# Performance work log

Measured on AMD Instinct MI355X. Metric: run time of the kernel, lower is better.

Reference implementation:

```python
import jax, jax.numpy as jnp
import numpy as np

NUM_NODES = 100000
NUM_EDGES = 1600000
NUM_GRAPHS = 512
HIDDEN = 128
LAYERS = 3
NUM_CLASSES = 10
BN_EPS = 1e-5


def setup_inputs() -> dict:
    key = jax.random.key(0)
    ks = jax.random.split(key, 12)
    x = jax.random.normal(ks[0], (NUM_NODES, HIDDEN), dtype=jnp.float32)
    edge_index = jax.random.randint(ks[1], (2, NUM_EDGES), 0, NUM_NODES, dtype=jnp.int32)
    batch = jnp.sort(jax.random.randint(ks[2], (NUM_NODES,), 0, NUM_GRAPHS, dtype=jnp.int32))
    s = 1.0 / np.sqrt(HIDDEN)
    W1 = jax.random.normal(ks[3], (LAYERS, HIDDEN, HIDDEN), dtype=jnp.float32) * s
    b1 = jnp.zeros((LAYERS, HIDDEN), dtype=jnp.float32)
    W2 = jax.random.normal(ks[4], (LAYERS, HIDDEN, HIDDEN), dtype=jnp.float32) * s
    b2 = jnp.zeros((LAYERS, HIDDEN), dtype=jnp.float32)
    gamma = jnp.ones((LAYERS, HIDDEN), dtype=jnp.float32)
    beta = jnp.zeros((LAYERS, HIDDEN), dtype=jnp.float32)
    eps_gin = jnp.zeros((LAYERS,), dtype=jnp.float32)  # train_eps init 0
    lin1_w = jax.random.normal(ks[5], (LAYERS * HIDDEN, HIDDEN), dtype=jnp.float32) * (1.0 / np.sqrt(LAYERS * HIDDEN))
    lin1_b = jnp.zeros((HIDDEN,), dtype=jnp.float32)
    lin2_w = jax.random.normal(ks[6], (HIDDEN, NUM_CLASSES), dtype=jnp.float32) * s
    lin2_b = jnp.zeros((NUM_CLASSES,), dtype=jnp.float32)
    return {"x": x, "edge_index": edge_index, "batch": batch,
            "W1": W1, "b1": b1, "W2": W2, "b2": b2,
            "gamma": gamma, "beta": beta, "eps_gin": eps_gin,
            "lin1_w": lin1_w, "lin1_b": lin1_b, "lin2_w": lin2_w, "lin2_b": lin2_b}


def _batchnorm(h, g, b):
    mu = jnp.mean(h, axis=0, keepdims=True)
    var = jnp.var(h, axis=0, keepdims=True)
    return (h - mu) * jax.lax.rsqrt(var + BN_EPS) * g + b


def reference(x, edge_index, batch, W1, b1, W2, b2, gamma, beta, eps_gin,
              lin1_w, lin1_b, lin2_w, lin2_b):
    src, dst = edge_index[0], edge_index[1]
    n = x.shape[0]
    h = x
    layer_hs = []
    for l in range(LAYERS):
        # scatter-add neighbor aggregation: agg[i] = sum_{j->i} h[j]
        agg = jax.ops.segment_sum(h[src], dst, num_segments=n)
        z = (1.0 + eps_gin[l]) * h + agg
        z = jax.nn.relu(z @ W1[l] + b1[l])
        z = jax.nn.relu(z @ W2[l] + b2[l])
        h = _batchnorm(z, gamma[l], beta[l])
        layer_hs.append(h)
    h_cat = jnp.concatenate(layer_hs, axis=-1)  # [N, LAYERS*HIDDEN]
    # global mean pool per graph
    sums = jax.ops.segment_sum(h_cat, batch, num_segments=NUM_GRAPHS)
    counts = jax.ops.segment_sum(jnp.ones((n, 1), h_cat.dtype), batch, num_segments=NUM_GRAPHS)
    g = sums / jnp.maximum(counts, 1.0)
    g = jax.nn.relu(g @ lin1_w + lin1_b)
    # dropout is identity in inference
    return g @ lin2_w + lin2_b
```

## Files before the change

### kernel.cpp

```cpp
#include <hip/hip_runtime.h>

#define HID 128
#define NGRAPH 512
#define NLAYERS 3
#define BN_EPS 1e-5f
#define NPB 256
#define EB 4096

typedef __attribute__((ext_vector_type(8))) short bf16x8;
typedef __attribute__((ext_vector_type(4))) float f32x4;
typedef __attribute__((ext_vector_type(2))) float f32x2;

__device__ inline unsigned short f2bf(float x) {
    union { float f; unsigned u; } v; v.f = x;
    unsigned r = v.u + 0x7FFFu + ((v.u >> 16) & 1u);
    return (unsigned short)(r >> 16);
}
__device__ inline float bf2f(unsigned short b) {
    union { float f; unsigned u; } v; v.u = ((unsigned)b) << 16; return v.f;
}
__device__ inline f32x2 bfp(unsigned u) {
    union { unsigned q; float f; } lo, hi;
    lo.q = u << 16; hi.q = u & 0xFFFF0000u;
    f32x2 r; r[0] = lo.f; r[1] = hi.f; return r;
}

__global__ void k_prep(float* __restrict__ ssliced, float* __restrict__ gsum,
                       const float4* __restrict__ x4, ushort* __restrict__ xb, int total4,
                       const float* __restrict__ W1, ushort* __restrict__ w1h, ushort* __restrict__ w1l,
                       const float* __restrict__ W2, ushort* __restrict__ w2h, ushort* __restrict__ w2l,
                       int wtotal, int xblocks,
                       const int* __restrict__ dst, int E, int* __restrict__ blkcnt) {
    __shared__ int hist[512];
    int b = blockIdx.x, t = threadIdx.x;
    if (b < 768) {
        if (b < 24) ssliced[b * 256 + t] = 0.0f;
        gsum[b * 256 + t] = 0.0f;
    } else if (b < 1152) {
        int gid = (b - 768) * 256 + t;
        const float* W; ushort *Wh, *Wl; int e;
        if (gid < wtotal) { W = W1; Wh = w1h; Wl = w1l; e = gid; }
        else              { W = W2; Wh = w2h; Wl = w2l; e = gid - wtotal; }
        if (e < wtotal) {
            int l = e >> 14, rem = e & 16383, k = rem >> 7, n = rem & 127;
            float v = W[e];
            ushort hi = f2bf(v);
            ushort lo = f2bf(v - bf2f(hi));
            int o = (l << 14) + (n << 7) + k;
            Wh[o] = hi; Wl[o] = lo;
        }
    } else if (b < 1152 + xblocks) {
        int i = (b - 1152) * 256 + t;
        if (i < total4) {
            float4 v = x4[i];
            uint2 p;
            p.x = ((unsigned)f2bf(v.y) << 16) | f2bf(v.x);
            p.y = ((unsigned)f2bf(v.w) << 16) | f2bf(v.z);
            ((uint2*)xb)[i] = p;
        }
    } else {
        int b2 = b - (1152 + xblocks);
        hist[t] = 0; hist[t + 256] = 0;
        __syncthreads();
        int base = b2 * EB;
        #pragma unroll
        for (int i = 0; i < 16; ++i) {
            int e = base + i * 256 + t;
            if (e < E) atomicAdd(&hist[dst[e] >> 8], 1);
        }
        __syncthreads();
        blkcnt[b2 * 512 + t]       = hist[t];
        blkcnt[b2 * 512 + t + 256] = hist[t + 256];
    }
}

__global__ __launch_bounds__(256) void k_btot_reduce(const int* __restrict__ blkcnt,
                                                     int eblk, int* __restrict__ tot) {
    __shared__ int sh[256];
    int b = blockIdx.x;
    int t = threadIdx.x;
    int s = 0;
    for (int j = t; j < eblk; j += 256) s += blkcnt[j * 512 + b];
    sh[t] = s;
    __syncthreads();
    #pragma unroll
    for (int k = 128; k > 0; k >>= 1) {
        if (t < k) sh[t] += sh[t + k];
        __syncthreads();
    }
    if (t == 0) tot[b] = sh[0];
}

__global__ __launch_bounds__(512) void k_bscan(const int* __restrict__ tot, int nb, int E,
                                               int* __restrict__ bbase, int* __restrict__ rowptrN) {
    __shared__ int sh[512];
    int t = threadIdx.x;
    sh[t] = (t < nb) ? tot[t] : 0;
    __syncthreads();
    #pragma unroll
    for (int s = 1; s < 512; s <<= 1) {
        int v = (t >= s) ? sh[t - s] : 0;
        __syncthreads();
        sh[t] += v;
        __syncthreads();
    }
    if (t < nb) bbase[t] = (t == 0) ? 0 : sh[t - 1];
    if (t == 0) { bbase[nb] = E; *rowptrN = E; }
}

__global__ __launch_bounds__(512) void k_colscan(int* __restrict__ blkcnt, int eblk,
                                                 const int* __restrict__ bbase) {
    __shared__ int sh[512];
    int t = threadIdx.x;
    int b = blockIdx.x;
    sh[t] = (t < eblk) ? blkcnt[t * 512 + b] : 0;
    __syncthreads();
    #pragma unroll
    for (int s = 1; s < 512; s <<= 1) {
        int v = (t >= s) ? sh[t - s] : 0;
        __syncthreads();
        sh[t] += v;
        __syncthreads();
    }
    int excl = (t == 0) ? 0 : sh[t - 1];
    if (t < eblk) blkcnt[t * 512 + b] = bbase[b] + excl;
}

__global__ __launch_bounds__(256) void k_bscatter(const int* __restrict__ src,
                                                  const int* __restrict__ dst, int E,
                                                  const int* __restrict__ blkcnt,
                                                  unsigned* __restrict__ pairs) {
    __shared__ int hist[512];
    __shared__ int lbase[512];
    int t = threadIdx.x;
    hist[t] = 0; hist[t + 256] = 0;
    lbase[t]       = blkcnt[blockIdx.x * 512 + t];
    lbase[t + 256] = blkcnt[blockIdx.x * 512 + t + 256];
    __syncthreads();
    int base = blockIdx.x * EB;
    #pragma unroll
    for (int i = 0; i < 16; ++i) {
        int e = base + i * 256 + t;
        if (e < E) {
            int d = dst[e];
            int b = d >> 8;
            int pos = lbase[b] + atomicAdd(&hist[b], 1);
            pairs[pos] = ((unsigned)(d & 255) << 24) | (unsigned)src[e];
        }
    }
}

__global__ __launch_bounds__(256) void k_bbuild(const unsigned* __restrict__ pairs,
                                                const int* __restrict__ bbase, int N,
                                                int* __restrict__ rowptr, int* __restrict__ csr) {
    __shared__ int cnt[256];
    __shared__ int off[256];
    int t = threadIdx.x;
    int b = blockIdx.x;
    int base = bbase[b], bcount = bbase[b + 1] - base;
    cnt[t] = 0;
    __syncthreads();
    for (int i = t; i < bcount; i += 256) atomicAdd(&cnt[pairs[base + i] >> 24], 1);
    __syncthreads();
    off[t] = cnt[t];
    __syncthreads();
    for (int s = 1; s < 256; s <<= 1) {
        int v = (t >= s) ? off[t - s] : 0;
        __syncthreads();
        off[t] += v;
        __syncthreads();
    }
    int excl = (t == 0) ? 0 : off[t - 1];
    int node = b * NPB + t;
    if (node < N) rowptr[node] = base + excl;
    cnt[t] = excl;
    __syncthreads();
    for (int i = t; i < bcount; i += 256) {
        unsigned p = pairs[base + i];
        int dl = p >> 24;
        int pos = base + atomicAdd(&cnt[dl], 1);
        csr[pos] = (int)(p & 0xFFFFFFu);
    }
}

__global__ __launch_bounds__(256, 8) void k_agg(
        const int* __restrict__ rowptr, const int* __restrict__ csr_src,
        const uint2* __restrict__ hinb,
        const float* __restrict__ prev_stats,
        const float* __restrict__ g_row, const float* __restrict__ be_row,
        const float* __restrict__ eps_gin, int layer,
        ushort* __restrict__ z0out, int N) {
    const int t = threadIdx.x;
    const int lane = t & 63;
    const int wv = t >> 6;
    const int q = lane >> 4;
    const int f = lane & 15;

    f32x2 scv2[4], shv2[4];
    if (prev_stats) {
        float invn = 1.0f / (float)N;
        #pragma unroll
        for (int d = 0; d < 4; ++d) {
            #pragma unroll
            for (int h = 0; h < 2; ++h) {
                int fi = f * 8 + d * 2 + h;
                float mu = prev_stats[fi] * invn;
                float var = prev_stats[128 + fi] * invn - mu * mu;
                float inv = rsqrtf(var + BN_EPS);
                float scj = g_row[fi] * inv;
                scv2[d][h] = scj; shv2[d][h] = be_row[fi] - mu * scj;
            }
        }
    } else {
        #pragma unroll
        for (int d = 0; d < 4; ++d) { scv2[d] = (f32x2){1.f, 1.f}; shv2[d] = (f32x2){0.f, 0.f}; }
    }
    float e1 = 1.0f + eps_gin[layer];
    const uint4* hin4 = (const uint4*)hinb;

    int r = blockIdx.x * 16 + wv * 4 + q;
    f32x2 a2[4];
    #pragma unroll
    for (int d = 0; d < 4; ++d) a2[d] = (f32x2){0.f, 0.f};
    float cdeg = 0.f;
    if (r < N) {
        int beg = rowptr[r], end = rowptr[r + 1];
        uint4 hv = hin4[(size_t)r * 16 + f];
        a2[0] = e1 * bfp(hv.x); a2[1] = e1 * bfp(hv.y);
        a2[2] = e1 * bfp(hv.z); a2[3] = e1 * bfp(hv.w);
        int p = beg;
        for (; p + 8 <= end; p += 8) {
            int s0 = csr_src[p],     s1 = csr_src[p + 1], s2 = csr_src[p + 2], s3 = csr_src[p + 3];
            int s4 = csr_src[p + 4], s5 = csr_src[p + 5], s6 = csr_src[p + 6], s7 = csr_src[p + 7];
            uint4 v0 = hin4[(size_t)s0 * 16 + f];
            uint4 v1 = hin4[(size_t)s1 * 16 + f];
            uint4 v2 = hin4[(size_t)s2 * 16 + f];
            uint4 v3 = hin4[(size_t)s3 * 16 + f];
            uint4 v4 = hin4[(size_t)s4 * 16 + f];
            uint4 v5 = hin4[(size_t)s5 * 16 + f];
            uint4 v6 = hin4[(size_t)s6 * 16 + f];
            uint4 v7 = hin4[(size_t)s7 * 16 + f];
            a2[0] += ((bfp(v0.x) + bfp(v1.x)) + (bfp(v2.x) + bfp(v3.x)))
                   + ((bfp(v4.x) + bfp(v5.x)) + (bfp(v6.x) + bfp(v7.x)));
            a2[1] += ((bfp(v0.y) + bfp(v1.y)) + (bfp(v2.y) + bfp(v3.y)))
                   + ((bfp(v4.y) + bfp(v5.y)) + (bfp(v6.y) + bfp(v7.y)));
            a2[2] += ((bfp(v0.z) + bfp(v1.z)) + (bfp(v2.z) + bfp(v3.z)))
                   + ((bfp(v4.z) + bfp(v5.z)) + (bfp(v6.z) + bfp(v7.z)));
            a2[3] += ((bfp(v0.w) + bfp(v1.w)) + (bfp(v2.w) + bfp(v3.w)))
                   + ((bfp(v4.w) + bfp(v5.w)) + (bfp(v6.w) + bfp(v7.w)));
        }
        if (p < end) {
            int last = end - 1;
            int c1 = min(p + 1, last), c2 = min(p + 2, last), c3 = min(p + 3, last);
            int c4 = min(p + 4, last), c5 = min(p + 5, last), c6 = min(p + 6, last);
            int s0 = csr_src[p],  s1 = csr_src[c1], s2 = csr_src[c2], s3 = csr_src[c3];
            int s4 = csr_src[c4], s5 = csr_src[c5], s6 = csr_src[c6];
            uint4 v0 = hin4[(size_t)s0 * 16 + f];
            uint4 v1 = hin4[(size_t)s1 * 16 + f];
            uint4 v2 = hin4[(size_t)s2 * 16 + f];
            uint4 v3 = hin4[(size_t)s3 * 16 + f];
            uint4 v4 = hin4[(size_t)s4 * 16 + f];
            uint4 v5 = hin4[(size_t)s5 * 16 + f];
            uint4 v6 = hin4[(size_t)s6 * 16 + f];
            int rem = end - p;
            unsigned m1 = (rem > 1) ? 0xFFFFFFFFu : 0u;
            unsigned m2 = (rem > 2) ? 0xFFFFFFFFu : 0u;
            unsigned m3 = (rem > 3) ? 0xFFFFFFFFu : 0u;
            unsigned m4 = (rem > 4) ? 0xFFFFFFFFu : 0u;
            unsigned m5 = (rem > 5) ? 0xFFFFFFFFu : 0u;
            unsigned m6 = (rem > 6) ? 0xFFFFFFFFu : 0u;
            a2[0] += ((bfp(v0.x) + bfp(v1.x & m1)) + (bfp(v2.x & m2) + bfp(v3.x & m3)))
                   + ((bfp(v4.x & m4) + bfp(v5.x & m5)) + bfp(v6.x & m6));
            a2[1] += ((bfp(v0.y) + bfp(v1.y & m1)) + (bfp(v2.y & m2) + bfp(v3.y & m3)))
                   + ((bfp(v4.y & m4) + bfp(v5.y & m5)) + bfp(v6.y & m6));
            a2[2] += ((bfp(v0.z) + bfp(v1.z & m1)) + (bfp(v2.z & m2) + bfp(v3.z & m3)))
                   + ((bfp(v4.z & m4) + bfp(v5.z & m5)) + bfp(v6.z & m6));
            a2[3] += ((bfp(v0.w) + bfp(v1.w & m1)) + (bfp(v2.w & m2) + bfp(v3.w & m3)))
                   + ((bfp(v4.w & m4) + bfp(v5.w & m5)) + bfp(v6.w & m6));
        }
        cdeg = e1 + (float)(end - beg);
    }
    f32x2 rr2[4];
    #pragma unroll
    for (int d = 0; d < 4; ++d) rr2[d] = scv2[d] * a2[d] + cdeg * shv2[d];
    uint4 ph;
    ph.x = ((unsigned)f2bf(rr2[0][1]) << 16) | f2bf(rr2[0][0]);
    ph.y = ((unsigned)f2bf(rr2[1][1]) << 16) | f2bf(rr2[1][0]);
    ph.z = ((unsigned)f2bf(rr2[2][1]) << 16) | f2bf(rr2[2][0]);
    ph.w = ((unsigned)f2bf(rr2[3][1]) << 16) | f2bf(rr2[3][0]);
    if (r < N) ((uint4*)z0out)[(size_t)r * 16 + f] = ph;
}

__global__ __launch_bounds__(256, 2) void k_mlp_dense(
        const uint4* __restrict__ z0, int layer, const int* __restrict__ batch,
        const ushort* __restrict__ w1h, const ushort* __restrict__ w1l,
        const float* __restrict__ b1,
        const ushort* __restrict__ w2h, const ushort* __restrict__ w2l,
        const float* __restrict__ b2,
        ushort* __restrict__ Hout, float* __restrict__ stat_sl,
        float* __restrict__ gsum, int N, int ntiles) {
    __shared__ __align__(16) ushort smem[8192];
    const int t = threadIdx.x;
    const int lane = t & 63;
    const int wv = t >> 6;
    const int li = lane & 15;
    const int kq = lane >> 4;
    const int n0 = wv * 32;
    const int swz = (li & 7) * 4;

    bf16x8 w1hr[8], w1lr[8], w2hr[8], w2lr[8];
    #pragma unroll
    for (int ch = 0; ch < 2; ++ch)
        #pragma unroll
        for (int ks = 0; ks < 2; ++ks)
            #pragma unroll
            for (int nt = 0; nt < 2; ++nt) {
                int i = ch * 4 + ks * 2 + nt;
                size_t wo = (size_t)(n0 + nt * 16 + li) * 128 + (ch * 64 + ks * 32 + kq * 8);
                w1hr[i] = *(const bf16x8*)&w1h[wo];
                w1lr[i] = *(const bf16x8*)&w1l[wo];
                w2hr[i] = *(const bf16x8*)&w2h[wo];
                w2lr[i] = *(const bf16x8*)&w2l[wo];
            }
    float bz0 = b1[n0 + li], bz1 = b1[n0 + 16 + li];
    float bb0 = b2[n0 + li], bb1 = b2[n0 + 16 + li];

    for (int tile = blockIdx.x; tile < ntiles; tile += gridDim.x) {
        const int row0 = tile * 64;

        {
            const uint4 zz = {0u, 0u, 0u, 0u};
            #pragma unroll
            for (int i = 0; i < 4; ++i) {
                int idx = i * 256 + t;
                int r = idx >> 4, f = idx & 15;
                uint4 v = (row0 + r < N) ? z0[(size_t)(row0 + r) * 16 + f] : zz;
                ((uint4*)smem)[r * 16 + (f ^ (r & 7))] = v;
            }
        }
        __syncthreads();

        f32x4 acc[4][2];
        #pragma unroll
        for (int i = 0; i < 4; ++i) {
            acc[i][0] = (f32x4){0.f, 0.f, 0.f, 0.f};
            acc[i][1] = (f32x4){0.f, 0.f, 0.f, 0.f};
        }

        #pragma unroll
        for (int ch = 0; ch < 2; ++ch) {
            #pragma unroll
            for (int ks = 0; ks < 2; ++ks) {
                int kcol = ch * 8 + ks * 4 + kq;
                #pragma unroll
                for (int mt = 0; mt < 4; ++mt) {
                    int r = mt * 16 + li;
                    int hw = (r * 16 + (kcol ^ (li & 7))) * 8;
                    bf16x8 ah = *(const bf16x8*)&smem[hw];
                    #pragma unroll
                    for (int nt = 0; nt < 2; ++nt) {
                        int i = ch * 4 + ks * 2 + nt;
                        acc[mt][nt] = __builtin_amdgcn_mfma_f32_16x16x32_bf16(ah, w1hr[i], acc[mt][nt], 0, 0, 0);
                        acc[mt][nt] = __builtin_amdgcn_mfma_f32_16x16x32_bf16(ah, w1lr[i], acc[mt][nt], 0, 0, 0);
                    }
                }
            }
        }

        __syncthreads();
        #pragma unroll
        for (int mt = 0; mt < 4; ++mt) {
            #pragma unroll
            for (int nt = 0; nt < 2; ++nt) {
                int c = n0 + nt * 16 + li;
                int dk = c >> 1;
                int halfbase = (dk >> 5) * 32;
                int dlow = dk & 31;
                int codd = c & 1;
                float bias = nt ? bz1 : bz0;
                #pragma unroll
                for (int reg = 0; reg < 4; ++reg) {
                    int r = mt * 16 + kq * 4 + reg;
                    float v = fmaxf(acc[mt][nt][reg] + bias, 0.f);
                    int us = (r * 64 + halfbase + (dlow ^ ((r & 7) * 4))) * 2 + codd;
                    smem[us] = f2bf(v);
                }
            }
        }
        #pragma unroll
        for (int i = 0; i < 4; ++i) {
            acc[i][0] = (f32x4){0.f, 0.f, 0.f, 0.f};
            acc[i][1] = (f32x4){0.f, 0.f, 0.f, 0.f};
        }
        __syncthreads();

        #pragma unroll
        for (int ch = 0; ch < 2; ++ch) {
            #pragma unroll
            for (int ks = 0; ks < 2; ++ks) {
                int aoff = (ks * 16 + kq * 4) ^ swz;
                #pragma unroll
                for (int mt = 0; mt < 4; ++mt) {
                    int idx = ((mt * 16 + li) * 64 + ch * 32 + aoff) * 2;
                    bf16x8 ah = *(const bf16x8*)&smem[idx];
                    #pragma unroll
                    for (int nt = 0; nt < 2; ++nt) {
                        int i = ch * 4 + ks * 2 + nt;
                        acc[mt][nt] = __builtin_amdgcn_mfma_f32_16x16x32_bf16(ah, w2hr[i], acc[mt][nt], 0, 0, 0);
                        acc[mt][nt] = __builtin_amdgcn_mfma_f32_16x16x32_bf16(ah, w2lr[i], acc[mt][nt], 0, 0, 0);
                    }
                }
            }
        }

        int btr[4][4];
        #pragma unroll
        for (int mt = 0; mt < 4; ++mt)
            #pragma unroll
            for (int reg = 0; reg < 4; ++reg) {
                int grow = row0 + mt * 16 + kq * 4 + reg;
                btr[mt][reg] = (grow < N) ? batch[grow] : -1;
            }
        __syncthreads();
        float s0 = 0.f, q0 = 0.f, s1 = 0.f, q1 = 0.f;
        #pragma unroll
        for (int mt = 0; mt < 4; ++mt) {
            #pragma unroll
            for (int reg = 0; reg < 4; ++reg) {
                int r = mt * 16 + kq * 4 + reg;
                float v0 = fmaxf(acc[mt][0][reg] + bb0, 0.f);
                float v1 = fmaxf(acc[mt][1][reg] + bb1, 0.f);
                smem[r * 128 + n0 + li]      = f2bf(v0);
                smem[r * 128 + n0 + 16 + li] = f2bf(v1);
                if (btr[mt][reg] >= 0) {
                    s0 += v0; q0 += v0 * v0; s1 += v1; q1 += v1 * v1;
                }
            }
        }
        __syncthreads();
        {
            int valid = N - row0; if (valid > 64) valid = 64;
            int tot = valid * 16;
            for (int i = t; i < tot; i += 256) {
                int r = i >> 4, c = i & 15;
                ((uint4*)&Hout[(size_t)(row0 + r) * HID])[c] = ((const uint4*)smem)[r * 16 + c];
            }
        }
        s0 += __shfl_xor(s0, 16); s0 += __shfl_xor(s0, 32);
        q0 += __shfl_xor(q0, 16); q0 += __shfl_xor(q0, 32);
        s1 += __shfl_xor(s1, 16); s1 += __shfl_xor(s1, 32);
        q1 += __shfl_xor(q1, 16); q1 += __shfl_xor(q1, 32);
        if (kq == 0) {
            float* ss = stat_sl + (blockIdx.x & 7) * 768;
            unsafeAtomicAdd(&ss[n0 + li], s0);
            unsafeAtomicAdd(&ss[128 + n0 + li], q0);
            unsafeAtomicAdd(&ss[n0 + 16 + li], s1);
            unsafeAtomicAdd(&ss[128 + n0 + 16 + li], q1);
        }
        int lastr = N - 1; if (lastr > row0 + 63) lastr = row0 + 63;
        int g_lo = batch[row0], g_hi = batch[lastr];
        int loff = layer * HID;
        for (int g = g_lo; g <= g_hi; ++g) {
            float p0 = 0.f, p1 = 0.f;
            #pragma unroll
            for (int mt = 0; mt < 4; ++mt)
                #pragma unroll
                for (int reg = 0; reg < 4; ++reg) {
                    if (btr[mt][reg] == g) {
                        p0 += fmaxf(acc[mt][0][reg] + bb0, 0.f);
                        p1 += fmaxf(acc[mt][1][reg] + bb1, 0.f);
                    }
                }
            p0 += __shfl_xor(p0, 16); p0 += __shfl_xor(p0, 32);
            p1 += __shfl_xor(p1, 16); p1 += __shfl_xor(p1, 32);
            if (kq == 0) {
                unsafeAtomicAdd(&gsum[(size_t)g * 384 + loff + n0 + li], p0);
                unsafeAtomicAdd(&gsum[(size_t)g * 384 + loff + n0 + 16 + li], p1);
            }
        }
        __syncthreads();
    }
}

__global__ __launch_bounds__(256) void k_sfold(const float* __restrict__ sliced,
                                               float* __restrict__ out) {
    int t = threadIdx.x;
    float s = 0.f;
    #pragma unroll
    for (int k = 0; k < 8; ++k) s += sliced[k * 768 + t];
    out[t] = s;
}

__global__ __launch_bounds__(128) void k_mlp(const int* __restrict__ batch, int N,
                     const float* __restrict__ gsum, const float* __restrict__ stats,
                     const float* __restrict__ gamma, const float* __restrict__ beta,
                     const float* __restrict__ w1, const float* __restrict__ b1,
                     const float* __restrict__ w2, const float* __restrict__ b2,
                     float* __restrict__ out) {
    __shared__ float gl[8][384];
    __shared__ float hh[8][128];
    int g0 = blockIdx.x * 8, t = threadIdx.x;
    float invn = 1.0f / (float)N;
    float sc[NLAYERS], sh[NLAYERS];
    #pragma unroll
    for (int l = 0; l < NLAYERS; ++l) {
        float mu = stats[l * 256 + t] * invn;
        float var = stats[l * 256 + 128 + t] * invn - mu * mu;
        float inv = rsqrtf(var + BN_EPS);
        sc[l] = gamma[l * HID + t] * inv;
        sh[l] = beta[l * HID + t] - mu * sc[l];
    }
    for (int j = 0; j < 8; ++j) {
        int g = g0 + j;
        int start, end;
        { int lo = 0, hi = N; while (lo < hi) { int m = (lo + hi) >> 1; if (batch[m] < g) lo = m + 1; else hi = m; } start = lo; }
        { int lo = start, hi = N; while (lo < hi) { int m = (lo + hi) >> 1; if (batch[m] < g + 1) lo = m + 1; else hi = m; } end = lo; }
        float cnt = (float)(end - start);
        float invc = 1.0f / fmaxf(cnt, 1.0f);
        #pragma unroll
        for (int l = 0; l < NLAYERS; ++l)
            gl[j][l * 128 + t] = (gsum[(size_t)g * 384 + l * 128 + t] * sc[l] + sh[l] * cnt) * invc;
    }
    __syncthreads();
    float acc[8];
    #pragma unroll
    for (int j = 0; j < 8; ++j) acc[j] = b1[t];
    for (int k = 0; k < 384; ++k) {
        float wv = w1[k * HID + t];
        #pragma unroll
        for (int j = 0; j < 8; ++j) acc[j] = fmaf(gl[j][k], wv, acc[j]);
    }
    #pragma unroll
    for (int j = 0; j < 8; ++j) hh[j][t] = fmaxf(acc[j], 0.f);
    __syncthreads();
    if (t < 80) {
        int j = t / 10, o = t % 10;
        float a2 = b2[o];
        for (int k = 0; k < 128; ++k) a2 = fmaf(hh[j][k], w2[k * 10 + o], a2);
        out[(g0 + j) * 10 + o] = a2;
    }
}

extern "C" void kernel_launch(void* const* d_in, const int* in_sizes, int n_in,
                              void* d_out, int out_size, void* d_ws, size_t ws_size,
                              hipStream_t stream) {
    const float* x     = (const float*)d_in[0];
    const int*   ei    = (const int*)d_in[1];
    const int*   batch = (const int*)d_in[2];
    const float* W1    = (const float*)d_in[3];
    const float* b1    = (const float*)d_in[4];
    const float* W2    = (const float*)d_in[5];
    const float* b2    = (const float*)d_in[6];
    const float* gamma = (const float*)d_in[7];
    const float* beta  = (const float*)d_in[8];
    const float* epsg  = (const float*)d_in[9];
    const float* l1w   = (const float*)d_in[10];
    const float* l1b   = (const float*)d_in[11];
    const float* l2w   = (const float*)d_in[12];
    const float* l2b   = (const float*)d_in[13];

    const int N = in_sizes[0] / HID;
    const int E = in_sizes[1] / 2;
    const int* src = ei;
    const int* dst = ei + E;
    const int nb = (N + NPB - 1) / NPB;
    const int eblk = (E + EB - 1) / EB;

    float* w = (float*)d_ws;
    const size_t NF = (size_t)N * HID;
    ushort* xb    = (ushort*)(w + NF);
    ushort* hb[3] = { xb + NF, xb + 2 * NF, xb + 3 * NF };
    ushort* z0buf = xb + 4 * NF;
    float* stats  = w + 4 * NF;
    float* sliced = stats + 768;
    float* gsum   = sliced + 6144;
    int*   rowptr = (int*)(gsum + (size_t)NGRAPH * 384);
    int*   csr    = rowptr + N + 1;
    int*   bbase  = csr + E;
    int*   btot   = bbase + nb + 2;
    ushort* wt  = (ushort*)(((uintptr_t)(btot + nb + 1) + 15) & ~(uintptr_t)15);
    ushort* w1h = wt;
    ushort* w1l = wt + 49152;
    ushort* w2h = wt + 98304;
    ushort* w2l = wt + 147456;

    unsigned* pairs  = (unsigned*)w;
    int*      blkcnt = (int*)(w + 2 * 1024 * 1024);

    const int total4 = (int)(NF / 4);
    const int xblocks = (total4 + 255) / 256;
    const int prep_blocks = 1152 + xblocks + eblk;
    k_prep<<<prep_blocks, 256, 0, stream>>>(sliced, gsum, (const float4*)x, xb, total4,
                                            W1, w1h, w1l, W2, w2h, w2l, NLAYERS * HID * HID,
                                            xblocks, dst, E, blkcnt);

    k_btot_reduce<<<nb, 256, 0, stream>>>(blkcnt, eblk, btot);
    k_bscan<<<1, 512, 0, stream>>>(btot, nb, E, bbase, rowptr + N);
    k_colscan<<<nb, 512, 0, stream>>>(blkcnt, eblk, bbase);
    k_bscatter<<<eblk, 256, 0, stream>>>(src, dst, E, blkcnt, pairs);
    k_bbuild<<<nb, 256, 0, stream>>>(pairs, bbase, N, rowptr, csr);

    const int ntiles = (N + 63) / 64;
    for (int l = 0; l < NLAYERS; ++l) {
        const ushort* hin = (l == 0) ? xb : hb[l - 1];
        const float* pstats = (l == 0) ? nullptr : (stats + (l - 1) * 256);
        const float* grow_  = gamma + (l == 0 ? 0 : (l - 1)) * HID;
        const float* brow_  = beta  + (l == 0 ? 0 : (l - 1)) * HID;

        k_agg<<<(N + 15) / 16, 256, 0, stream>>>(
            rowptr, csr, (const uint2*)hin, pstats, grow_, brow_, epsg, l, z0buf, N);

        k_mlp_dense<<<512, 256, 0, stream>>>(
            (const uint4*)z0buf, l, batch,
            w1h + (size_t)l * 16384, w1l + (size_t)l * 16384, b1 + l * HID,
            w2h + (size_t)l * 16384, w2l + (size_t)l * 16384, b2 + l * HID,
            hb[l], sliced + l * 256, gsum, N, ntiles);

        k_sfold<<<1, 256, 0, stream>>>(sliced + l * 256, stats + l * 256);
    }

    k_mlp<<<NGRAPH / 8, 128, 0, stream>>>(batch, N, gsum, stats, gamma, beta,
                                          l1w, l1b, l2w, l2b, (float*)d_out);
}
```

Before: 602.2 us.

## Cut kernel launches: fold stats reductions, atomic bucket totals, one-tile-per-block MLP

Removes the k_btot_reduce and per-layer k_sfold kernels. Bucket totals are now accumulated with global atomics inside k_prep, and the sliced BN statistics are folded inside k_agg and k_mlp, which cuts launch and serialization overhead. Zeroing of gsum/sliced/btot moves to a hipMemsetAsync. k_mlp_dense drops its persistent tile loop and launches one block per 64-row tile, which reloads the weight registers in every block. k_agg's occupancy bound is lowered from 8 to 6 waves.

```diff
diff --git a/kernel.cpp b/kernel.cpp
--- a/kernel.cpp
+++ b/kernel.cpp
@@ -25,19 +25,16 @@
     f32x2 r; r[0] = lo.f; r[1] = hi.f; return r;
 }
 
-__global__ void k_prep(float* __restrict__ ssliced, float* __restrict__ gsum,
-                       const float4* __restrict__ x4, ushort* __restrict__ xb, int total4,
+__global__ void k_prep(const float4* __restrict__ x4, ushort* __restrict__ xb, int total4,
                        const float* __restrict__ W1, ushort* __restrict__ w1h, ushort* __restrict__ w1l,
                        const float* __restrict__ W2, ushort* __restrict__ w2h, ushort* __restrict__ w2l,
                        int wtotal, int xblocks,
-                       const int* __restrict__ dst, int E, int* __restrict__ blkcnt) {
+                       const int* __restrict__ dst, int E, int* __restrict__ blkcnt,
+                       int* __restrict__ btot) {
     __shared__ int hist[512];
     int b = blockIdx.x, t = threadIdx.x;
-    if (b < 768) {
-        if (b < 24) ssliced[b * 256 + t] = 0.0f;
-        gsum[b * 256 + t] = 0.0f;
-    } else if (b < 1152) {
-        int gid = (b - 768) * 256 + t;
+    if (b < 384) {
+        int gid = b * 256 + t;
         const float* W; ushort *Wh, *Wl; int e;
         if (gid < wtotal) { W = W1; Wh = w1h; Wl = w1l; e = gid; }
         else              { W = W2; Wh = w2h; Wl = w2l; e = gid - wtotal; }
@@ -49,8 +46,8 @@
             int o = (l << 14) + (n << 7) + k;
             Wh[o] = hi; Wl[o] = lo;
         }
-    } else if (b < 1152 + xblocks) {
-        int i = (b - 1152) * 256 + t;
+    } else if (b < 384 + xblocks) {
+        int i = (b - 384) * 256 + t;
         if (i < total4) {
             float4 v = x4[i];
             uint2 p;
@@ -59,7 +56,7 @@
             ((uint2*)xb)[i] = p;
         }
     } else {
-        int b2 = b - (1152 + xblocks);
+        int b2 = b - (384 + xblocks);
         hist[t] = 0; hist[t + 256] = 0;
         __syncthreads();
         int base = b2 * EB;
@@ -71,24 +68,9 @@
         __syncthreads();
         blkcnt[b2 * 512 + t]       = hist[t];
         blkcnt[b2 * 512 + t + 256] = hist[t + 256];
-    }
-}
-
-__global__ __launch_bounds__(256) void k_btot_reduce(const int* __restrict__ blkcnt,
-                                                     int eblk, int* __restrict__ tot) {
-    __shared__ int sh[256];
-    int b = blockIdx.x;
-    int t = threadIdx.x;
-    int s = 0;
-    for (int j = t; j < eblk; j += 256) s += blkcnt[j * 512 + b];
-    sh[t] = s;
-    __syncthreads();
-    #pragma unroll
-    for (int k = 128; k > 0; k >>= 1) {
-        if (t < k) sh[t] += sh[t + k];
-        __syncthreads();
-    }
-    if (t == 0) tot[b] = sh[0];
+        if (hist[t])       atomicAdd(&btot[t], hist[t]);
+        if (hist[t + 256]) atomicAdd(&btot[t + 256], hist[t + 256]);
+    }
 }
 
 __global__ __launch_bounds__(512) void k_bscan(const int* __restrict__ tot, int nb, int E,
@@ -183,29 +165,38 @@
     }
 }
 
-__global__ __launch_bounds__(256, 8) void k_agg(
+__global__ __launch_bounds__(256, 6) void k_agg(
         const int* __restrict__ rowptr, const int* __restrict__ csr_src,
         const uint2* __restrict__ hinb,
-        const float* __restrict__ prev_stats,
+        const float* __restrict__ prev_sliced,
         const float* __restrict__ g_row, const float* __restrict__ be_row,
         const float* __restrict__ eps_gin, int layer,
         ushort* __restrict__ z0out, int N) {
+    __shared__ float sfold[256];
     const int t = threadIdx.x;
     const int lane = t & 63;
     const int wv = t >> 6;
     const int q = lane >> 4;
     const int f = lane & 15;
 
+    if (prev_sliced) {
+        float s = 0.f;
+        #pragma unroll
+        for (int k = 0; k < 8; ++k) s += prev_sliced[k * 768 + t];
+        sfold[t] = s;
+        __syncthreads();
+    }
+
     f32x2 scv2[4], shv2[4];
-    if (prev_stats) {
+    if (prev_sliced) {
         float invn = 1.0f / (float)N;
         #pragma unroll
         for (int d = 0; d < 4; ++d) {
             #pragma unroll
             for (int h = 0; h < 2; ++h) {
                 int fi = f * 8 + d * 2 + h;
-                float mu = prev_stats[fi] * invn;
-                float var = prev_stats[128 + fi] * invn - mu * mu;
+                float mu = sfold[fi] * invn;
+                float var = sfold[128 + fi] * invn - mu * mu;
                 float inv = rsqrtf(var + BN_EPS);
                 float scj = g_row[fi] * inv;
                 scv2[d][h] = scj; shv2[d][h] = be_row[fi] - mu * scj;
@@ -298,7 +289,7 @@
         const ushort* __restrict__ w2h, const ushort* __restrict__ w2l,
         const float* __restrict__ b2,
         ushort* __restrict__ Hout, float* __restrict__ stat_sl,
-        float* __restrict__ gsum, int N, int ntiles) {
+        float* __restrict__ gsum, int N) {
     __shared__ __align__(16) ushort smem[8192];
     const int t = threadIdx.x;
     const int lane = t & 63;
@@ -306,6 +297,7 @@
     const int li = lane & 15;
     const int kq = lane >> 4;
     const int n0 = wv * 32;
+    const int row0 = blockIdx.x * 64;
     const int swz = (li & 7) * 4;
 
     bf16x8 w1hr[8], w1lr[8], w2hr[8], w2lr[8];
@@ -322,177 +314,163 @@
                 w2hr[i] = *(const bf16x8*)&w2h[wo];
                 w2lr[i] = *(const bf16x8*)&w2l[wo];
             }
-    float bz0 = b1[n0 + li], bz1 = b1[n0 + 16 + li];
-    float bb0 = b2[n0 + li], bb1 = b2[n0 + 16 + li];
-
-    for (int tile = blockIdx.x; tile < ntiles; tile += gridDim.x) {
-        const int row0 = tile * 64;
-
-        {
-            const uint4 zz = {0u, 0u, 0u, 0u};
+
+    {
+        const uint4 zz = {0u, 0u, 0u, 0u};
+        #pragma unroll
+        for (int i = 0; i < 4; ++i) {
+            int idx = i * 256 + t;
+            int r = idx >> 4, f = idx & 15;
+            uint4 v = (row0 + r < N) ? z0[(size_t)(row0 + r) * 16 + f] : zz;
+            ((uint4*)smem)[r * 16 + (f ^ (r & 7))] = v;
+        }
+    }
+    __syncthreads();
+
+    f32x4 acc[4][2];
+    #pragma unroll
+    for (int i = 0; i < 4; ++i) {
+        acc[i][0] = (f32x4){0.f, 0.f, 0.f, 0.f};
+        acc[i][1] = (f32x4){0.f, 0.f, 0.f, 0.f};
+    }
+
+    #pragma unroll
+    for (int ch = 0; ch < 2; ++ch) {
+        #pragma unroll
+        for (int ks = 0; ks < 2; ++ks) {
+            int kcol = ch * 8 + ks * 4 + kq;
             #pragma unroll
-            for (int i = 0; i < 4; ++i) {
-                int idx = i * 256 + t;
-                int r = idx >> 4, f = idx & 15;
-                uint4 v = (row0 + r < N) ? z0[(size_t)(row0 + r) * 16 + f] : zz;
-                ((uint4*)smem)[r * 16 + (f ^ (r & 7))] = v;
-            }
-        }
-        __syncthreads();
-
-        f32x4 acc[4][2];
-        #pragma unroll
-        for (int i = 0; i < 4; ++i) {
-            acc[i][0] = (f32x4){0.f, 0.f, 0.f, 0.f};
-            acc[i][1] = (f32x4){0.f, 0.f, 0.f, 0.f};
-        }
-
-        #pragma unroll
-        for (int ch = 0; ch < 2; ++ch) {
-            #pragma unroll
-            for (int ks = 0; ks < 2; ++ks) {
-                int kcol = ch * 8 + ks * 4 + kq;
+            for (int mt = 0; mt < 4; ++mt) {
+                int r = mt * 16 + li;
+                int hw = (r * 16 + (kcol ^ (li & 7))) * 8;
+                bf16x8 ah = *(const bf16x8*)&smem[hw];
                 #pragma unroll
-                for (int mt = 0; mt < 4; ++mt) {
-                    int r = mt * 16 + li;
-                    int hw = (r * 16 + (kcol ^ (li & 7))) * 8;
-                    bf16x8 ah = *(const bf16x8*)&smem[hw];
-                    #pragma unroll
-                    for (int nt = 0; nt < 2; ++nt) {
-                        int i = ch * 4 + ks * 2 + nt;
-                        acc[mt][nt] = __builtin_amdgcn_mfma_f32_16x16x32_bf16(ah, w1hr[i], acc[mt][nt], 0, 0, 0);
-                        acc[mt][nt] = __builtin_amdgcn_mfma_f32_16x16x32_bf16(ah, w1lr[i], acc[mt][nt], 0, 0, 0);
-                    }
+                for (int nt = 0; nt < 2; ++nt) {
+                    int i = ch * 4 + ks * 2 + nt;
+                    acc[mt][nt] = __builtin_amdgcn_mfma_f32_16x16x32_bf16(ah, w1hr[i], acc[mt][nt], 0, 0, 0);
+                    acc[mt][nt] = __builtin_amdgcn_mfma_f32_16x16x32_bf16(ah, w1lr[i], acc[mt][nt], 0, 0, 0);
                 }
             }
         }
-
-        __syncthreads();
-        #pragma unroll
-        for (int mt = 0; mt < 4; ++mt) {
+    }
+
+    float bz0 = b1[n0 + li], bz1 = b1[n0 + 16 + li];
+    __syncthreads();
+    #pragma unroll
+    for (int mt = 0; mt < 4; ++mt) {
+        #pragma unroll
+        for (int nt = 0; nt < 2; ++nt) {
+            int c = n0 + nt * 16 + li;
+            int dk = c >> 1;
+            int halfbase = (dk >> 5) * 32;
+            int dlow = dk & 31;
+            int codd = c & 1;
+            float bias = nt ? bz1 : bz0;
             #pragma unroll
-            for (int nt = 0; nt < 2; ++nt) {
-                int c = n0 + nt * 16 + li;
-                int dk = c >> 1;
-                int halfbase = (dk >> 5) * 32;
-                int dlow = dk & 31;
-                int codd = c & 1;
-                float bias = nt ? bz1 : bz0;
+            for (int reg = 0; reg < 4; ++reg) {
+                int r = mt * 16 + kq * 4 + reg;
+                float v = fmaxf(acc[mt][nt][reg] + bias, 0.f);
+                int us = (r * 64 + halfbase + (dlow ^ ((r & 7) * 4))) * 2 + codd;
+                smem[us] = f2bf(v);
+            }
+        }
+    }
+    #pragma unroll
+    for (int i = 0; i < 4; ++i) {
+        acc[i][0] = (f32x4){0.f, 0.f, 0.f, 0.f};
+        acc[i][1] = (f32x4){0.f, 0.f, 0.f, 0.f};
+    }
+    __syncthreads();
+
+    #pragma unroll
+    for (int ch = 0; ch < 2; ++ch) {
+        #pragma unroll
+        for (int ks = 0; ks < 2; ++ks) {
+            int aoff = (ks * 16 + kq * 4) ^ swz;
+            #pragma unroll
+            for (int mt = 0; mt < 4; ++mt) {
+                int idx = ((mt * 16 + li) * 64 + ch * 32 + aoff) * 2;
+                bf16x8 ah = *(const bf16x8*)&smem[idx];
                 #pragma unroll
-                for (int reg = 0; reg < 4; ++reg) {
-                    int r = mt * 16 + kq * 4 + reg;
-                    float v = fmaxf(acc[mt][nt][reg] + bias, 0.f);
-                    int us = (r * 64 + halfbase + (dlow ^ ((r & 7) * 4))) * 2 + codd;
-                    smem[us] = f2bf(v);
+                for (int nt = 0; nt < 2; ++nt) {
+                    int i = ch * 4 + ks * 2 + nt;
+                    acc[mt][nt] = __builtin_amdgcn_mfma_f32_16x16x32_bf16(ah, w2hr[i], acc[mt][nt], 0, 0, 0);
+                    acc[mt][nt] = __builtin_amdgcn_mfma_f32_16x16x32_bf16(ah, w2lr[i], acc[mt][nt], 0, 0, 0);
                 }
             }
         }
-        #pragma unroll
-        for (int i = 0; i < 4; ++i) {
-            acc[i][0] = (f32x4){0.f, 0.f, 0.f, 0.f};
-            acc[i][1] = (f32x4){0.f, 0.f, 0.f, 0.f};
-        }
-        __syncthreads();
-
-        #pragma unroll
-        for (int ch = 0; ch < 2; ++ch) {
-            #pragma unroll
-            for (int ks = 0; ks < 2; ++ks) {
-                int aoff = (ks * 16 + kq * 4) ^ swz;
-                #pragma unroll
-                for (int mt = 0; mt < 4; ++mt) {
-                    int idx = ((mt * 16 + li) * 64 + ch * 32 + aoff) * 2;
-                    bf16x8 ah = *(const bf16x8*)&smem[idx];
-                    #pragma unroll
-                    for (int nt = 0; nt < 2; ++nt) {
-                        int i = ch * 4 + ks * 2 + nt;
-                        acc[mt][nt] = __builtin_amdgcn_mfma_f32_16x16x32_bf16(ah, w2hr[i], acc[mt][nt], 0, 0, 0);
-                        acc[mt][nt] = __builtin_amdgcn_mfma_f32_16x16x32_bf16(ah, w2lr[i], acc[mt][nt], 0, 0, 0);
-                    }
-                }
+    }
+
+    float bb0 = b2[n0 + li], bb1 = b2[n0 + 16 + li];
+    int btr[4][4];
+    #pragma unroll
+    for (int mt = 0; mt < 4; ++mt)
+        #pragma unroll
+        for (int reg = 0; reg < 4; ++reg) {
+            int grow = row0 + mt * 16 + kq * 4 + reg;
+            btr[mt][reg] = (grow < N) ? batch[grow] : -1;
+        }
+    __syncthreads();
+    float s0 = 0.f, q0 = 0.f, s1 = 0.f, q1 = 0.f;
+    #pragma unroll
+    for (int mt = 0; mt < 4; ++mt) {
+        #pragma unroll
+        for (int reg = 0; reg < 4; ++reg) {
+            int r = mt * 16 + kq * 4 + reg;
+            float v0 = fmaxf(acc[mt][0][reg] + bb0, 0.f);
+            float v1 = fmaxf(acc[mt][1][reg] + bb1, 0.f);
+            smem[r * 128 + n0 + li]      = f2bf(v0);
+            smem[r * 128 + n0 + 16 + li] = f2bf(v1);
+            if (btr[mt][reg] >= 0) {
+                s0 += v0; q0 += v0 * v0; s1 += v1; q1 += v1 * v1;
             }
         }
-
-        int btr[4][4];
+    }
+    __syncthreads();
+    {
+        int valid = N - row0; if (valid > 64) valid = 64;
+        int tot = valid * 16;
+        for (int i = t; i < tot; i += 256) {
+            int r = i >> 4, c = i & 15;
+            ((uint4*)&Hout[(size_t)(row0 + r) * HID])[c] = ((const uint4*)smem)[r * 16 + c];
+        }
+    }
+    s0 += __shfl_xor(s0, 16); s0 += __shfl_xor(s0, 32);
+    q0 += __shfl_xor(q0, 16); q0 += __shfl_xor(q0, 32);
+    s1 += __shfl_xor(s1, 16); s1 += __shfl_xor(s1, 32);
+    q1 += __shfl_xor(q1, 16); q1 += __shfl_xor(q1, 32);
+    if (kq == 0) {
+        float* ss = stat_sl + (blockIdx.x & 7) * 768;
+        unsafeAtomicAdd(&ss[n0 + li], s0);
+        unsafeAtomicAdd(&ss[128 + n0 + li], q0);
+        unsafeAtomicAdd(&ss[n0 + 16 + li], s1);
+        unsafeAtomicAdd(&ss[128 + n0 + 16 + li], q1);
+    }
+    int lastr = N - 1; if (lastr > row0 + 63) lastr = row0 + 63;
+    int g_lo = batch[row0], g_hi = batch[lastr];
+    int loff = layer * HID;
+    for (int g = g_lo; g <= g_hi; ++g) {
+        float p0 = 0.f, p1 = 0.f;
         #pragma unroll
         for (int mt = 0; mt < 4; ++mt)
             #pragma unroll
             for (int reg = 0; reg < 4; ++reg) {
-                int grow = row0 + mt * 16 + kq * 4 + reg;
-                btr[mt][reg] = (grow < N) ? batch[grow] : -1;
-            }
-        __syncthreads();
-        float s0 = 0.f, q0 = 0.f, s1 = 0.f, q1 = 0.f;
-        #pragma unroll
-        for (int mt = 0; mt < 4; ++mt) {
-            #pragma unroll
-            for (int reg = 0; reg < 4; ++reg) {
-                int r = mt * 16 + kq * 4 + reg;
-                float v0 = fmaxf(acc[mt][0][reg] + bb0, 0.f);
-                float v1 = fmaxf(acc[mt][1][reg] + bb1, 0.f);
-                smem[r * 128 + n0 + li]      = f2bf(v0);
-                smem[r * 128 + n0 + 16 + li] = f2bf(v1);
-                if (btr[mt][reg] >= 0) {
-                    s0 += v0; q0 += v0 * v0; s1 += v1; q1 += v1 * v1;
+                if (btr[mt][reg] == g) {
+                    p0 += fmaxf(acc[mt][0][reg] + bb0, 0.f);
+                    p1 += fmaxf(acc[mt][1][reg] + bb1, 0.f);
                 }
             }
-        }
-        __syncthreads();
-        {
-            int valid = N - row0; if (valid > 64) valid = 64;
-            int tot = valid * 16;
-            for (int i = t; i < tot; i += 256) {
-                int r = i >> 4, c = i & 15;
-                ((uint4*)&Hout[(size_t)(row0 + r) * HID])[c] = ((const uint4*)smem)[r * 16 + c];
-            }
-        }
-        s0 += __shfl_xor(s0, 16); s0 += __shfl_xor(s0, 32);
-        q0 += __shfl_xor(q0, 16); q0 += __shfl_xor(q0, 32);
-        s1 += __shfl_xor(s1, 16); s1 += __shfl_xor(s1, 32);
-        q1 += __shfl_xor(q1, 16); q1 += __shfl_xor(q1, 32);
+        p0 += __shfl_xor(p0, 16); p0 += __shfl_xor(p0, 32);
+        p1 += __shfl_xor(p1, 16); p1 += __shfl_xor(p1, 32);
         if (kq == 0) {
-            float* ss = stat_sl + (blockIdx.x & 7) * 768;
-            unsafeAtomicAdd(&ss[n0 + li], s0);
-            unsafeAtomicAdd(&ss[128 + n0 + li], q0);
-            unsafeAtomicAdd(&ss[n0 + 16 + li], s1);
-            unsafeAtomicAdd(&ss[128 + n0 + 16 + li], q1);
-        }
-        int lastr = N - 1; if (lastr > row0 + 63) lastr = row0 + 63;
-        int g_lo = batch[row0], g_hi = batch[lastr];
-        int loff = layer * HID;
-        for (int g = g_lo; g <= g_hi; ++g) {
-            float p0 = 0.f, p1 = 0.f;
-            #pragma unroll
-            for (int mt = 0; mt < 4; ++mt)
-                #pragma unroll
-                for (int reg = 0; reg < 4; ++reg) {
-                    if (btr[mt][reg] == g) {
-                        p0 += fmaxf(acc[mt][0][reg] + bb0, 0.f);
-                        p1 += fmaxf(acc[mt][1][reg] + bb1, 0.f);
-                    }
-                }
-            p0 += __shfl_xor(p0, 16); p0 += __shfl_xor(p0, 32);
-            p1 += __shfl_xor(p1, 16); p1 += __shfl_xor(p1, 32);
-            if (kq == 0) {
-                unsafeAtomicAdd(&gsum[(size_t)g * 384 + loff + n0 + li], p0);
-                unsafeAtomicAdd(&gsum[(size_t)g * 384 + loff + n0 + 16 + li], p1);
-            }
-        }
-        __syncthreads();
-    }
-}
-
-__global__ __launch_bounds__(256) void k_sfold(const float* __restrict__ sliced,
-                                               float* __restrict__ out) {
-    int t = threadIdx.x;
-    float s = 0.f;
-    #pragma unroll
-    for (int k = 0; k < 8; ++k) s += sliced[k * 768 + t];
-    out[t] = s;
+            unsafeAtomicAdd(&gsum[(size_t)g * 384 + loff + n0 + li], p0);
+            unsafeAtomicAdd(&gsum[(size_t)g * 384 + loff + n0 + 16 + li], p1);
+        }
+    }
 }
 
 __global__ __launch_bounds__(128) void k_mlp(const int* __restrict__ batch, int N,
-                     const float* __restrict__ gsum, const float* __restrict__ stats,
+                     const float* __restrict__ gsum, const float* __restrict__ sliced,
                      const float* __restrict__ gamma, const float* __restrict__ beta,
                      const float* __restrict__ w1, const float* __restrict__ b1,
                      const float* __restrict__ w2, const float* __restrict__ b2,
@@ -504,8 +482,14 @@
     float sc[NLAYERS], sh[NLAYERS];
     #pragma unroll
     for (int l = 0; l < NLAYERS; ++l) {
-        float mu = stats[l * 256 + t] * invn;
-        float var = stats[l * 256 + 128 + t] * invn - mu * mu;
+        float sum_ = 0.f, sq_ = 0.f;
+        #pragma unroll
+        for (int k = 0; k < 8; ++k) {
+            sum_ += sliced[k * 768 + l * 256 + t];
+            sq_  += sliced[k * 768 + l * 256 + 128 + t];
+        }
+        float mu = sum_ * invn;
+        float var = sq_ * invn - mu * mu;
         float inv = rsqrtf(var + BN_EPS);
         sc[l] = gamma[l * HID + t] * inv;
         sh[l] = beta[l * HID + t] - mu * sc[l];
@@ -571,14 +555,13 @@
     ushort* xb    = (ushort*)(w + NF);
     ushort* hb[3] = { xb + NF, xb + 2 * NF, xb + 3 * NF };
     ushort* z0buf = xb + 4 * NF;
-    float* stats  = w + 4 * NF;
-    float* sliced = stats + 768;
+    float* sliced = w + 4 * NF;
     float* gsum   = sliced + 6144;
-    int*   rowptr = (int*)(gsum + (size_t)NGRAPH * 384);
+    int*   btot   = (int*)(gsum + (size_t)NGRAPH * 384);
+    int*   rowptr = btot + 513;
     int*   csr    = rowptr + N + 1;
     int*   bbase  = csr + E;
-    int*   btot   = bbase + nb + 2;
-    ushort* wt  = (ushort*)(((uintptr_t)(btot + nb + 1) + 15) & ~(uintptr_t)15);
+    ushort* wt  = (ushort*)(((uintptr_t)(bbase + nb + 2) + 15) & ~(uintptr_t)15);
     ushort* w1h = wt;
     ushort* w1l = wt + 49152;
     ushort* w2h = wt + 98304;
@@ -587,38 +570,36 @@
     unsigned* pairs  = (unsigned*)w;
     int*      blkcnt = (int*)(w + 2 * 1024 * 1024);
 
+    hipMemsetAsync(sliced, 0, (6144 + (size_t)NGRAPH * 384 + 513) * sizeof(float), stream);
+
     const int total4 = (int)(NF / 4);
     const int xblocks = (total4 + 255) / 256;
-    const int prep_blocks = 1152 + xblocks + eblk;
-    k_prep<<<prep_blocks, 256, 0, stream>>>(sliced, gsum, (const float4*)x, xb, total4,
+    const int prep_blocks = 384 + xblocks + eblk;
+    k_prep<<<prep_blocks, 256, 0, stream>>>((const float4*)x, xb, total4,
                                             W1, w1h, w1l, W2, w2h, w2l, NLAYERS * HID * HID,
-                                            xblocks, dst, E, blkcnt);
-
-    k_btot_reduce<<<nb, 256, 0, stream>>>(blkcnt, eblk, btot);
+                                            xblocks, dst, E, blkcnt, btot);
+
     k_bscan<<<1, 512, 0, stream>>>(btot, nb, E, bbase, rowptr + N);
     k_colscan<<<nb, 512, 0, stream>>>(blkcnt, eblk, bbase);
     k_bscatter<<<eblk, 256, 0, stream>>>(src, dst, E, blkcnt, pairs);
     k_bbuild<<<nb, 256, 0, stream>>>(pairs, bbase, N, rowptr, csr);
 
-    const int ntiles = (N + 63) / 64;
     for (int l = 0; l < NLAYERS; ++l) {
         const ushort* hin = (l == 0) ? xb : hb[l - 1];
-        const float* pstats = (l == 0) ? nullptr : (stats + (l - 1) * 256);
+        const float* psl    = (l == 0) ? nullptr : (sliced + (l - 1) * 256);
         const float* grow_  = gamma + (l == 0 ? 0 : (l - 1)) * HID;
         const float* brow_  = beta  + (l == 0 ? 0 : (l - 1)) * HID;
 
         k_agg<<<(N + 15) / 16, 256, 0, stream>>>(
-            rowptr, csr, (const uint2*)hin, pstats, grow_, brow_, epsg, l, z0buf, N);
-
-        k_mlp_dense<<<512, 256, 0, stream>>>(
+            rowptr, csr, (const uint2*)hin, psl, grow_, brow_, epsg, l, z0buf, N);
+
+        k_mlp_dense<<<(N + 63) / 64, 256, 0, stream>>>(
             (const uint4*)z0buf, l, batch,
             w1h + (size_t)l * 16384, w1l + (size_t)l * 16384, b1 + l * HID,
             w2h + (size_t)l * 16384, w2l + (size_t)l * 16384, b2 + l * HID,
-            hb[l], sliced + l * 256, gsum, N, ntiles);
-
-        k_sfold<<<1, 256, 0, stream>>>(sliced + l * 256, stats + l * 256);
-    }
-
-    k_mlp<<<NGRAPH / 8, 128, 0, stream>>>(batch, N, gsum, stats, gamma, beta,
+            hb[l], sliced + l * 256, gsum, N);
+    }
+
+    k_mlp<<<NGRAPH / 8, 128, 0, stream>>>(batch, N, gsum, sliced, gamma, beta,
                                           l1w, l1b, l2w, l2b, (float*)d_out);
 }
```

New measurement: 562.3 us. -6.6%, faster.
